# Kernel tuning notes

Hardware: AMD Instinct MI355X
Metric: run time of the kernel (lower is better)

The kernel has to match this reference:

```python
import jax, jax.numpy as jnp
import numpy as np

P = 8  # hard-coded patch size in DCTFFN

def dct_matrix(n):
    # get_dctMatrix: orthonormal DCT-II basis
    j = np.arange(n)
    i = np.arange(n).reshape(-1, 1)
    C = np.cos(np.pi * i * (2 * j + 1) / (2 * n)) * np.sqrt(2.0 / n)
    C[0, :] = np.sqrt(1.0 / n)
    return jnp.asarray(C, dtype=jnp.float32)

def setup_inputs():
    key = jax.random.key(0)
    ks = jax.random.split(key, 4)
    dim, hidden = 64, 170
    x = jax.random.normal(ks[0], (4, dim, 256, 256), jnp.float32)
    W_in = jax.random.normal(ks[1], (2 * hidden, dim), jnp.float32) * 0.05
    W_dw = jax.random.normal(ks[2], (2 * hidden, 1, 3, 3), jnp.float32) * 0.1
    quant = jnp.ones((2 * hidden, 1, 1, P, P), jnp.float32)
    W_out = jax.random.normal(ks[3], (dim, hidden), jnp.float32) * 0.05
    return dict(x=x, W_in=W_in, W_dw=W_dw, quant=quant, W_out=W_out)

def reference(x, W_in, W_dw, quant, W_out):
    M = dct_matrix(P)  # [8,8], used for both H and W axes (patch is square)
    # project_in: 1x1 conv, no bias
    y = jnp.einsum('oc,bchw->bohw', W_in, x)
    b, c2, h, w = y.shape
    ph = (P - h % P) % P
    pw = (P - w % P) % P
    if ph or pw:
        y = jnp.pad(y, ((0, 0), (0, 0), (0, ph), (0, pw)), mode='reflect')
    H, W = y.shape[-2:]
    # b c (h p1) (w p2) -> b c h w p1 p2
    xp = y.reshape(b, c2, H // P, P, W // P, P).transpose(0, 1, 2, 4, 3, 5)
    # 2D DCT per 8x8 patch: Y = M @ X @ M^T
    xd = jnp.einsum('ip,bchwpq,jq->bchwij', M, xp, M)
    xd = xd * quant  # learned frequency scaling, broadcast over (h, w)
    # 2D IDCT: Y = M^T @ X @ M
    xi = jnp.einsum('pi,bchwpq,qj->bchwij', M, xd, M)
    # back to b c H W, crop padding
    yr = xi.transpose(0, 1, 2, 4, 3, 5).reshape(b, c2, H, W)[:, :, :h, :w]
    # depthwise 3x3 conv, padding=1, no bias
    dw = jax.lax.conv_general_dilated(
        yr, W_dw, window_strides=(1, 1), padding=((1, 1), (1, 1)),
        dimension_numbers=('NCHW', 'OIHW', 'NCHW'), feature_group_count=c2)
    x1, x2 = jnp.split(dw, 2, axis=1)
    g = jax.nn.gelu(x1, approximate=False) * x2
    # project_out: 1x1 conv, no bias
    return jnp.einsum('oc,bchw->bohw', W_out, g)
```

## Files before the change

kernel.cpp:

```cpp
#include <hip/hip_runtime.h>
#include <cmath>

#define HW   256
#define NPIX 65536
#define NP   65600
#define CIN  64
#define C2   340
#define HID  170

typedef _Float16 f16x8 __attribute__((ext_vector_type(8)));
typedef float    f32x4 __attribute__((ext_vector_type(4)));
typedef unsigned int u32;

#define A0 0.35355339059327373f
#define A1 0.49039264020161522f
#define A2 0.46193976625564337f
#define A3 0.41573480615127262f
#define A4 0.35355339059327379f
#define A5 0.27778511650980114f
#define A6 0.19134171618254492f
#define A7 0.09754516100806417f

__device__ __forceinline__ void dct8(const float v[8], float y[8]) {
    const float u0 = v[0] + v[7], u1 = v[1] + v[6];
    const float u2 = v[2] + v[5], u3 = v[3] + v[4];
    const float w0 = v[0] - v[7], w1 = v[1] - v[6];
    const float w2 = v[2] - v[5], w3 = v[3] - v[4];
    const float s0 = u0 + u3, s1 = u1 + u2;
    const float t0 = u0 - u3, t1 = u1 - u2;
    y[0] = A0 * (s0 + s1);
    y[4] = A4 * (s0 - s1);
    y[2] = fmaf(A2, t0,  A6 * t1);
    y[6] = fmaf(A6, t0, -A2 * t1);
    y[1] = fmaf(A1, w0, fmaf( A3, w1, fmaf( A5, w2,  A7 * w3)));
    y[3] = fmaf(A3, w0, fmaf(-A7, w1, fmaf(-A1, w2, -A5 * w3)));
    y[5] = fmaf(A5, w0, fmaf(-A1, w1, fmaf( A7, w2,  A3 * w3)));
    y[7] = fmaf(A7, w0, fmaf(-A5, w1, fmaf( A3, w2, -A1 * w3)));
}

__device__ __forceinline__ void idct8(const float y[8], float x[8]) {
    const float sa = fmaf( A4, y[4], A0 * y[0]);
    const float sb = fmaf(-A4, y[4], A0 * y[0]);
    const float c0 = fmaf( A2, y[2],  A6 * y[6]);
    const float c1 = fmaf( A6, y[2], -A2 * y[6]);
    const float e0 = sa + c0, e3 = sa - c0;
    const float e1 = sb + c1, e2 = sb - c1;
    const float o0 = fmaf(A1, y[1], fmaf( A3, y[3], fmaf( A5, y[5],  A7 * y[7])));
    const float o1 = fmaf(A3, y[1], fmaf(-A7, y[3], fmaf(-A1, y[5], -A5 * y[7])));
    const float o2 = fmaf(A5, y[1], fmaf(-A1, y[3], fmaf( A7, y[5],  A3 * y[7])));
    const float o3 = fmaf(A7, y[1], fmaf(-A5, y[3], fmaf( A3, y[5], -A1 * y[7])));
    x[0] = e0 + o0; x[7] = e0 - o0;
    x[1] = e1 + o1; x[6] = e1 - o1;
    x[2] = e2 + o2; x[5] = e2 - o2;
    x[3] = e3 + o3; x[4] = e3 - o3;
}

__device__ __forceinline__ int pcolrot(int blk, int row, int ocl) {
    return ((blk + row + (ocl >> 2)) & 3) << 3;
}

__global__ __launch_bounds__(256) void kprep(const float* __restrict__ Win,
                                             const float* __restrict__ Wout,
                                             _Float16* __restrict__ WinH,
                                             _Float16* __restrict__ WoutKH)
{
    const int i = blockIdx.x * 256 + threadIdx.x;
    if (i < 352 * 64) WinH[i] = (i < C2 * 64) ? (_Float16)Win[i] : (_Float16)0.f;
    if (i < 64 * 192) {
        const int o = i / 192, h = i - o * 192;
        WoutKH[i] = (h < HID) ? (_Float16)Wout[o * HID + h] : (_Float16)0.f;
    }
}

__global__ __launch_bounds__(256) void kA(
    const float* __restrict__ x,
    const _Float16* __restrict__ WinH,
    const float* __restrict__ quant,
    _Float16* __restrict__ yr)
{
    const int tid  = threadIdx.x;
    const int tile = blockIdx.x;
    const int bb   = blockIdx.y;
    const int ty = tile >> 3, tx = tile & 7;
    const int y0 = ty * 8,    x0 = tx * 32;
    const int wv = tid >> 6;
    const int l15 = tid & 15, quad = (tid & 63) >> 4;

    __shared__ float csh[32 * 264];

    if (tile == 0) {
        const f16x8 z = {(_Float16)0.f,(_Float16)0.f,(_Float16)0.f,(_Float16)0.f,
                         (_Float16)0.f,(_Float16)0.f,(_Float16)0.f,(_Float16)0.f};
#pragma unroll 1
        for (int it = 0; it < 11; ++it) {
            const int idx = tid + it * 256;
            if (idx < C2 * 8) {
                const int oc = idx >> 3, sub = idx & 7;
                *(f16x8*)&yr[(size_t)(bb * C2 + oc) * NP + NPIX + sub * 8] = z;
            }
        }
    }

    const int ch  = tid >> 5;
    const int pat = (tid >> 3) & 3;
    const int lan = tid & 7;

    const float* xb = x + (size_t)bb * (CIN * NPIX);

    f16x8 af0[4], af1[4];
#pragma unroll
    for (int hh = 0; hh < 2; ++hh) {
#pragma unroll
        for (int di = 0; di < 4; ++di) {
            const int ci = ch + 8 * di;
            const float* gp = xb + (size_t)(hh * 32 + ci) * NPIX
                              + (y0 + lan) * HW + x0 + pat * 8;
            float v[8], o[8];
            *(f32x4*)&v[0] = *(const f32x4*)gp;
            *(f32x4*)&v[4] = *(const f32x4*)(gp + 4);
            dct8(v, o);
            float* rowp = &csh[ci * 264 + lan * 32 + pcolrot(pat, lan, ci)];
            *(f32x4*)rowp       = *(const f32x4*)&o[0];
            *(f32x4*)(rowp + 4) = *(const f32x4*)&o[4];
        }
        __syncthreads();
#pragma unroll
        for (int di = 0; di < 4; ++di) {
            const int ci = ch + 8 * di;
            float v[8], o[8];
#pragma unroll
            for (int i = 0; i < 8; ++i)
                v[i] = csh[ci * 264 + i * 32 + pcolrot(pat, i, ci) + lan];
            dct8(v, o);
#pragma unroll
            for (int i = 0; i < 8; ++i)
                csh[ci * 264 + i * 32 + pcolrot(pat, i, ci) + lan] = o[i];
        }
        __syncthreads();
#pragma unroll
        for (int tt = 0; tt < 4; ++tt) {
            const int apx = (wv * 4 + tt) * 16 + l15;
            const int prw = apx >> 5;
            const int pc  = apx & 31;
            const int pp  = pc >> 3, pl = pc & 7;
            union { _Float16 h[8]; f16x8 v; } pk;
#pragma unroll
            for (int e = 0; e < 8; ++e) {
                const int ci = quad * 8 + e;
                pk.h[e] = (_Float16)csh[ci * 264 + prw * 32
                                        + pcolrot(pp, prw, ci) + pl];
            }
            if (hh == 0) af0[tt] = pk.v; else af1[tt] = pk.v;
        }
        __syncthreads();
    }

#pragma unroll 1
    for (int sc = 0; sc < 11; ++sc) {
        const int oc0 = sc * 32;

#pragma unroll
        for (int g2 = 0; g2 < 2; ++g2) {
            const int ocb = oc0 + g2 * 16 + l15;
            const f16x8 b0 = *(const f16x8*)(WinH + ocb * 64 + quad * 8);
            const f16x8 b1 = *(const f16x8*)(WinH + ocb * 64 + 32 + quad * 8);
            const int ocl = g2 * 16 + l15;
            int ocq = oc0 + ocl; if (ocq > C2 - 1) ocq = C2 - 1;
            const float* qbase = quant + ocq * 64 + (quad & 1) * 4;
#pragma unroll
            for (int tt = 0; tt < 4; ++tt) {
                const int tile16 = wv * 4 + tt;
                f32x4 acc = {0.f, 0.f, 0.f, 0.f};
                acc = __builtin_amdgcn_mfma_f32_16x16x32_f16(af0[tt], b0, acc, 0, 0, 0);
                acc = __builtin_amdgcn_mfma_f32_16x16x32_f16(af1[tt], b1, acc, 0, 0, 0);
                const int prow = tile16 >> 1;
                const int blk  = ((tile16 & 1) << 1) | (quad >> 1);
                const f32x4 qv = *(const f32x4*)(qbase + prow * 8);
                acc *= qv;
                *(f32x4*)&csh[ocl * 264 + prow * 32 + pcolrot(blk, prow, ocl)
                              + (quad & 1) * 4] = acc;
            }
        }
        __syncthreads();

#pragma unroll
        for (int di = 0; di < 4; ++di) {
            const int ocl = ch + 8 * di;
            float v[8], e8[8];
#pragma unroll
            for (int i = 0; i < 8; ++i)
                v[i] = csh[ocl * 264 + i * 32 + pcolrot(pat, i, ocl) + lan];
            idct8(v, e8);
#pragma unroll
            for (int i = 0; i < 8; ++i)
                csh[ocl * 264 + i * 32 + pcolrot(pat, i, ocl) + lan] = e8[i];
        }
        __syncthreads();

#pragma unroll
        for (int di = 0; di < 4; ++di) {
            const int ocl = ch + 8 * di;
            const int oc  = oc0 + ocl;
            const float* rowp = &csh[ocl * 264 + lan * 32 + pcolrot(pat, lan, ocl)];
            float v[8], e8[8];
            *(f32x4*)&v[0] = *(const f32x4*)rowp;
            *(f32x4*)&v[4] = *(const f32x4*)(rowp + 4);
            idct8(v, e8);
            union { _Float16 h[8]; f16x8 f; } u;
#pragma unroll
            for (int q = 0; q < 8; ++q) u.h[q] = (_Float16)e8[q];
            if (oc < C2) {
                f16x8* dst = (f16x8*)(yr + (size_t)(bb * C2 + oc) * NP
                                      + (y0 + lan) * HW + x0 + pat * 8);
                *dst = u.f;
            }
        }
        __syncthreads();
    }
}

__global__ __launch_bounds__(256, 2) void kB(
    const _Float16* __restrict__ yr,
    const float* __restrict__ Wdw,
    const _Float16* __restrict__ WoutKH,
    float* __restrict__ out)
{
    const int tid = threadIdx.x;
    const int bb  = blockIdx.y;
    const int id  = blockIdx.x;
    const int row = ((id & 7) << 5) | (id >> 3);
    const int wv  = tid >> 6;
    const int L   = tid & 63;
    const int l15 = tid & 15, quad = (tid & 63) >> 4;

    __shared__ union {
        _Float16 g[256 * 32];
        float    t[16 * 257];
    } shm;

    const char* ybase = (const char*)(yr + (size_t)bb * C2 * NP) - 16;

    unsigned boff[3];
#pragma unroll
    for (int rr = 0; rr < 3; ++rr) {
        const int trow = row + rr - 1;
        boff[rr] = ((unsigned)trow < (unsigned)HW)
                 ? (unsigned)(trow * (HW * 2) + 8 * L + 12)
                 : (unsigned)(NPIX * 2 + 16);
    }
    const float mL = (L == 0)  ? 0.f : 1.f;
    const float mR = (L == 63) ? 0.f : 1.f;

    f32x4 acc[4][4];
#pragma unroll
    for (int a = 0; a < 4; ++a)
#pragma unroll
        for (int b = 0; b < 4; ++b) acc[a][b] = (f32x4){0.f, 0.f, 0.f, 0.f};

    char* gpc = (char*)shm.g + L * 256 + ((wv ^ (L & 3)) << 4);

#pragma unroll 1
    for (int chunk = 0; chunk < 6; ++chunk) {
        const int hc = chunk * 32;

        union { _Float16 h[8]; f16x8 v; } pk0, pk1, pk2, pk3;
#pragma unroll
        for (int j = 0; j < 8; ++j) {
            const int h = hc + wv * 8 + j;
            float gg0 = 0.f, gg1 = 0.f, gg2 = 0.f, gg3 = 0.f;
            if (h < HID) {
                const char* p1 = ybase + (size_t)h * (NP * 2);
                const char* p2 = p1 + (size_t)HID * (NP * 2);
                const float* w1 = Wdw + h * 9;
                const float* w2 = w1 + HID * 9;
                float s1[4] = {0.f, 0.f, 0.f, 0.f};
                float s2[4] = {0.f, 0.f, 0.f, 0.f};
#pragma unroll
                for (int rr = 0; rr < 3; ++rr) {
                    f16x8 a1, a2;
                    __builtin_memcpy(&a1, p1 + boff[rr], 16);
                    __builtin_memcpy(&a2, p2 + boff[rr], 16);
                    float v1[8], v2[8];
#pragma unroll
                    for (int e = 1; e <= 6; ++e) {
                        v1[e] = (float)a1[e];
                        v2[e] = (float)a2[e];
                    }
                    v1[1] *= mL; v2[1] *= mL;
                    v1[6] *= mR; v2[6] *= mR;
                    const float wa = w1[rr*3+0], wb = w1[rr*3+1], wc = w1[rr*3+2];
                    const float wd = w2[rr*3+0], we = w2[rr*3+1], wf = w2[rr*3+2];
#pragma unroll
                    for (int i = 0; i < 4; ++i) {
                        s1[i] = fmaf(v1[i+1], wa, s1[i]);
                        s1[i] = fmaf(v1[i+2], wb, s1[i]);
                        s1[i] = fmaf(v1[i+3], wc, s1[i]);
                        s2[i] = fmaf(v2[i+1], wd, s2[i]);
                        s2[i] = fmaf(v2[i+2], we, s2[i]);
                        s2[i] = fmaf(v2[i+3], wf, s2[i]);
                    }
                }
                const float KC = 0.70710678118654752f;
                gg0 = 0.5f * s1[0] * (1.f + erff(s1[0] * KC)) * s2[0];
                gg1 = 0.5f * s1[1] * (1.f + erff(s1[1] * KC)) * s2[1];
                gg2 = 0.5f * s1[2] * (1.f + erff(s1[2] * KC)) * s2[2];
                gg3 = 0.5f * s1[3] * (1.f + erff(s1[3] * KC)) * s2[3];
            }
            pk0.h[j] = (_Float16)gg0;
            pk1.h[j] = (_Float16)gg1;
            pk2.h[j] = (_Float16)gg2;
            pk3.h[j] = (_Float16)gg3;
        }
        *(f16x8*)(gpc      ) = pk0.v;
        *(f16x8*)(gpc +  64) = pk1.v;
        *(f16x8*)(gpc + 128) = pk2.v;
        *(f16x8*)(gpc + 192) = pk3.v;
        __syncthreads();

#pragma unroll
        for (int tt = 0; tt < 4; ++tt) {
            const int apx = (wv * 4 + tt) * 16 + l15;
            const f16x8 a = *(const f16x8*)((const char*)shm.g + apx * 64
                              + ((quad ^ ((l15 >> 2) & 3)) << 4));
#pragma unroll
            for (int p = 0; p < 4; ++p) {
                const f16x8 b = *(const f16x8*)(WoutKH + (p * 16 + l15) * 192 + hc + quad * 8);
                acc[tt][p] = __builtin_amdgcn_mfma_f32_16x16x32_f16(a, b, acc[tt][p], 0, 0, 0);
            }
        }
        __syncthreads();
    }

    float* ob = out + (size_t)bb * CIN * NPIX + row * HW + tid;
#pragma unroll
    for (int p = 0; p < 4; ++p) {
#pragma unroll
        for (int tt = 0; tt < 4; ++tt) {
            const int px = (wv * 4 + tt) * 16 + quad * 4;
#pragma unroll
            for (int reg = 0; reg < 4; ++reg)
                shm.t[l15 * 257 + px + reg] = acc[tt][p][reg];
        }
        __syncthreads();
#pragma unroll
        for (int o2 = 0; o2 < 16; ++o2)
            ob[(size_t)(p * 16 + o2) * NPIX] = shm.t[o2 * 257 + tid];
        __syncthreads();
    }
}

extern "C" void kernel_launch(void* const* d_in, const int* in_sizes, int n_in,
                              void* d_out, int out_size, void* d_ws, size_t ws_size,
                              hipStream_t stream)
{
    const float* x     = (const float*)d_in[0];
    const float* Win   = (const float*)d_in[1];
    const float* Wdw   = (const float*)d_in[2];
    const float* quant = (const float*)d_in[3];
    const float* Wout  = (const float*)d_in[4];
    float* out = (float*)d_out;

    _Float16* WinH   = (_Float16*)d_ws;
    _Float16* WoutKH = (_Float16*)((char*)d_ws + 45056);
    _Float16* yrbuf  = (_Float16*)((char*)d_ws + 69632);

    const size_t perBatch = (size_t)C2 * NP * sizeof(_Float16);
    const size_t head = 69632;
    const size_t avail = ws_size > head ? ws_size - head : 0;
    int nb = 1;
    if (avail >= 4 * perBatch)      nb = 4;
    else if (avail >= 2 * perBatch) nb = 2;

    kprep<<<88, 256, 0, stream>>>(Win, Wout, WinH, WoutKH);

    for (int b0 = 0; b0 < 4; b0 += nb) {
        dim3 grid(256, nb);
        kA<<<grid, 256, 0, stream>>>(x + (size_t)b0 * CIN * NPIX, WinH, quant, yrbuf);
        kB<<<grid, 256, 0, stream>>>(yrbuf, Wdw, WoutKH, out + (size_t)b0 * CIN * NPIX);
    }
}
```

Before: 309.2 us.

## Split depthwise-conv/GELU stage from project-out GEMM into separate kernels via global buffer

The fused kB kernel is split into kG, which computes the depthwise 3x3 conv and GELU gating and writes the fp16 gated activations to a global workspace buffer in an MFMA-friendly swizzled layout, and kB2, which reads that buffer and runs the project-out MFMA GEMM. kG uses twice as many blocks, each doing half the hidden chunks, and both kernels raise launch bounds to 4 blocks per CU. The goal is better occupancy and latency hiding by removing the per-chunk LDS staging and barriers. The cost is an extra global write and read of about 25 MB per batch, plus a larger workspace that may reduce how many batches run per launch.

```diff
diff --git a/kernel.cpp b/kernel.cpp
--- a/kernel.cpp
+++ b/kernel.cpp
@@ -7,6 +7,9 @@
 #define CIN  64
 #define C2   340
 #define HID  170
+
+#define GROWB   98304
+#define GBATCH  (256 * (size_t)GROWB)
 
 typedef _Float16 f16x8 __attribute__((ext_vector_type(8)));
 typedef float    f32x4 __attribute__((ext_vector_type(4)));
@@ -219,24 +222,19 @@
     }
 }
 
-__global__ __launch_bounds__(256, 2) void kB(
+__global__ __launch_bounds__(256, 4) void kG(
     const _Float16* __restrict__ yr,
     const float* __restrict__ Wdw,
-    const _Float16* __restrict__ WoutKH,
-    float* __restrict__ out)
+    _Float16* __restrict__ g)
 {
-    const int tid = threadIdx.x;
-    const int bb  = blockIdx.y;
-    const int id  = blockIdx.x;
-    const int row = ((id & 7) << 5) | (id >> 3);
-    const int wv  = tid >> 6;
-    const int L   = tid & 63;
-    const int l15 = tid & 15, quad = (tid & 63) >> 4;
-
-    __shared__ union {
-        _Float16 g[256 * 32];
-        float    t[16 * 257];
-    } shm;
+    const int tid  = threadIdx.x;
+    const int bb   = blockIdx.y;
+    const int idf  = blockIdx.x;
+    const int id   = idf & 255;
+    const int half = idf >> 8;
+    const int row  = ((id & 7) << 5) | (id >> 3);
+    const int wv   = tid >> 6;
+    const int L    = tid & 63;
 
     const char* ybase = (const char*)(yr + (size_t)bb * C2 * NP) - 16;
 
@@ -251,16 +249,11 @@
     const float mL = (L == 0)  ? 0.f : 1.f;
     const float mR = (L == 63) ? 0.f : 1.f;
 
-    f32x4 acc[4][4];
-#pragma unroll
-    for (int a = 0; a < 4; ++a)
-#pragma unroll
-        for (int b = 0; b < 4; ++b) acc[a][b] = (f32x4){0.f, 0.f, 0.f, 0.f};
-
-    char* gpc = (char*)shm.g + L * 256 + ((wv ^ (L & 3)) << 4);
+    char* gbase = (char*)g + (size_t)bb * GBATCH + (size_t)row * GROWB
+                + L * 256 + ((wv ^ (L & 3)) << 4);
 
 #pragma unroll 1
-    for (int chunk = 0; chunk < 6; ++chunk) {
+    for (int chunk = half * 3; chunk < half * 3 + 3; ++chunk) {
         const int hc = chunk * 32;
 
         union { _Float16 h[8]; f16x8 v; } pk0, pk1, pk2, pk3;
@@ -311,24 +304,56 @@
             pk2.h[j] = (_Float16)gg2;
             pk3.h[j] = (_Float16)gg3;
         }
-        *(f16x8*)(gpc      ) = pk0.v;
-        *(f16x8*)(gpc +  64) = pk1.v;
-        *(f16x8*)(gpc + 128) = pk2.v;
-        *(f16x8*)(gpc + 192) = pk3.v;
-        __syncthreads();
-
+        char* gp = gbase + chunk * 16384;
+        *(f16x8*)(gp      ) = pk0.v;
+        *(f16x8*)(gp +  64) = pk1.v;
+        *(f16x8*)(gp + 128) = pk2.v;
+        *(f16x8*)(gp + 192) = pk3.v;
+    }
+}
+
+__global__ __launch_bounds__(256, 4) void kB2(
+    const _Float16* __restrict__ g,
+    const _Float16* __restrict__ WoutKH,
+    float* __restrict__ out)
+{
+    const int tid = threadIdx.x;
+    const int bb  = blockIdx.y;
+    const int id  = blockIdx.x;
+    const int row = ((id & 7) << 5) | (id >> 3);
+    const int wv  = tid >> 6;
+    const int l15 = tid & 15, quad = (tid & 63) >> 4;
+
+    __shared__ float tsh[16 * 257];
+
+    const char* gb = (const char*)g + (size_t)bb * GBATCH + (size_t)row * GROWB;
+    const int slotoff = (quad ^ ((l15 >> 2) & 3)) << 4;
+
+    f32x4 acc[4][4];
+#pragma unroll
+    for (int a = 0; a < 4; ++a)
+#pragma unroll
+        for (int b = 0; b < 4; ++b) acc[a][b] = (f32x4){0.f, 0.f, 0.f, 0.f};
+
+#pragma unroll 1
+    for (int chunk = 0; chunk < 6; ++chunk) {
+        const int hc = chunk * 32;
+        const char* gc = gb + chunk * 16384;
+
+        f16x8 av[4];
 #pragma unroll
         for (int tt = 0; tt < 4; ++tt) {
             const int apx = (wv * 4 + tt) * 16 + l15;
-            const f16x8 a = *(const f16x8*)((const char*)shm.g + apx * 64
-                              + ((quad ^ ((l15 >> 2) & 3)) << 4));
+            __builtin_memcpy(&av[tt], gc + apx * 64 + slotoff, 16);
+        }
+#pragma unroll
+        for (int tt = 0; tt < 4; ++tt) {
 #pragma unroll
             for (int p = 0; p < 4; ++p) {
                 const f16x8 b = *(const f16x8*)(WoutKH + (p * 16 + l15) * 192 + hc + quad * 8);
-                acc[tt][p] = __builtin_amdgcn_mfma_f32_16x16x32_f16(a, b, acc[tt][p], 0, 0, 0);
-            }
-        }
-        __syncthreads();
+                acc[tt][p] = __builtin_amdgcn_mfma_f32_16x16x32_f16(av[tt], b, acc[tt][p], 0, 0, 0);
+            }
+        }
     }
 
     float* ob = out + (size_t)bb * CIN * NPIX + row * HW + tid;
@@ -339,12 +364,12 @@
             const int px = (wv * 4 + tt) * 16 + quad * 4;
 #pragma unroll
             for (int reg = 0; reg < 4; ++reg)
-                shm.t[l15 * 257 + px + reg] = acc[tt][p][reg];
+                tsh[l15 * 257 + px + reg] = acc[tt][p][reg];
         }
         __syncthreads();
 #pragma unroll
         for (int o2 = 0; o2 < 16; ++o2)
-            ob[(size_t)(p * 16 + o2) * NPIX] = shm.t[o2 * 257 + tid];
+            ob[(size_t)(p * 16 + o2) * NPIX] = tsh[o2 * 257 + tid];
         __syncthreads();
     }
 }
@@ -364,18 +389,23 @@
     _Float16* WoutKH = (_Float16*)((char*)d_ws + 45056);
     _Float16* yrbuf  = (_Float16*)((char*)d_ws + 69632);
 
-    const size_t perBatch = (size_t)C2 * NP * sizeof(_Float16);
+    const size_t yrB  = (size_t)C2 * NP * sizeof(_Float16);
+    const size_t gB   = GBATCH;
+    const size_t perBatch = yrB + gB;
     const size_t head = 69632;
     const size_t avail = ws_size > head ? ws_size - head : 0;
     int nb = 1;
     if (avail >= 4 * perBatch)      nb = 4;
     else if (avail >= 2 * perBatch) nb = 2;
 
+    _Float16* gbuf = (_Float16*)((char*)d_ws + head + (size_t)nb * yrB);
+
     kprep<<<88, 256, 0, stream>>>(Win, Wout, WinH, WoutKH);
 
     for (int b0 = 0; b0 < 4; b0 += nb) {
-        dim3 grid(256, nb);
-        kA<<<grid, 256, 0, stream>>>(x + (size_t)b0 * CIN * NPIX, WinH, quant, yrbuf);
-        kB<<<grid, 256, 0, stream>>>(yrbuf, Wdw, WoutKH, out + (size_t)b0 * CIN * NPIX);
-    }
-}
+        dim3 gridA(256, nb), gridG(512, nb), gridB(256, nb);
+        kA<<<gridA, 256, 0, stream>>>(x + (size_t)b0 * CIN * NPIX, WinH, quant, yrbuf);
+        kG<<<gridG, 256, 0, stream>>>(yrbuf, Wdw, gbuf);
+        kB2<<<gridB, 256, 0, stream>>>(gbuf, WoutKH, out + (size_t)b0 * CIN * NPIX);
+    }
+}
```

Result: slower. 363.3 us (+17.5%).
